# Kernel tuning notes

Hardware: AMD Instinct MI355X
Metric: run time of the kernel (lower is better)

The kernel has to match this reference:

```python
import jax, jax.numpy as jnp
import numpy as np

B, S, TEXT_DIM, VISION_DIM, HIDDEN, HEADS = 4, 2048, 768, 768, 512, 8
HEAD_DIM = HIDDEN // HEADS


def setup_inputs() -> dict:
    key = jax.random.key(0)
    ks = jax.random.split(key, 9)
    s_in = 1.0 / np.sqrt(TEXT_DIM)
    s_h = 1.0 / np.sqrt(HIDDEN)
    return {
        "text_embeds": jax.random.normal(ks[0], (B, S, TEXT_DIM), dtype=jnp.float32),
        "Wq": jax.random.uniform(ks[1], (TEXT_DIM, HIDDEN), jnp.float32, -s_in, s_in),
        "bq": jax.random.uniform(ks[2], (HIDDEN,), jnp.float32, -s_in, s_in),
        "Wk": jax.random.uniform(ks[3], (TEXT_DIM, HIDDEN), jnp.float32, -s_in, s_in),
        "bk": jax.random.uniform(ks[4], (HIDDEN,), jnp.float32, -s_in, s_in),
        "Wv": jax.random.uniform(ks[5], (TEXT_DIM, HIDDEN), jnp.float32, -s_in, s_in),
        "bv": jax.random.uniform(ks[6], (HIDDEN,), jnp.float32, -s_in, s_in),
        "Wo": jax.random.uniform(ks[7], (HIDDEN, VISION_DIM), jnp.float32, -s_h, s_h),
        "bo": jax.random.uniform(ks[8], (VISION_DIM,), jnp.float32, -s_h, s_h),
    }


def reference(text_embeds, Wq, bq, Wk, bk, Wv, bv, Wo, bo):
    b, s, _ = text_embeds.shape
    # QKV projections -> [b, heads, s, head_dim]
    def proj(W, bias):
        y = jnp.einsum("bsd,dh->bsh", text_embeds, W) + bias
        return y.reshape(b, s, HEADS, HEAD_DIM).transpose(0, 2, 1, 3)
    q, k, v = proj(Wq, bq), proj(Wk, bk), proj(Wv, bv)
    scores = jnp.einsum("bhqd,bhkd->bhqk", q, k) / np.sqrt(HEAD_DIM).astype(np.float32)
    weights = jax.nn.softmax(scores, axis=-1)
    attended = jnp.einsum("bhqk,bhkd->bhqd", weights, v)
    attended = attended.transpose(0, 2, 1, 3).reshape(b, s, HIDDEN)
    out = jnp.einsum("bsh,hv->bsv", attended, Wo) + bo
    return jnp.squeeze(out, axis=1) if out.shape[1] == 1 else out
```

## Files before the change

### kernel.cpp

```cpp
#include <hip/hip_runtime.h>
#include <hip/hip_bf16.h>

#define BATCH 4
#define SEQ 2048
#define TDIM 768
#define VDIM 768
#define HID 512
#define NHEADS 8
#define HDIM 64
#define MROWS (BATCH * SEQ)
#define NQKV (3 * HID)

typedef unsigned short ushort_t;
typedef __attribute__((ext_vector_type(8))) short short8;
typedef __attribute__((ext_vector_type(4))) short short4v;
typedef __attribute__((ext_vector_type(4))) float floatx4;

#define QSCALE 0.18033688011112042f

__device__ __forceinline__ ushort_t bf16_rne(float f) {
    unsigned int u = __float_as_uint(f);
    u = (u + 0x7fffu + ((u >> 16) & 1u)) >> 16;
    return (ushort_t)u;
}

__device__ __forceinline__ void async16(const ushort_t* g, ushort_t* l) {
    __builtin_amdgcn_global_load_lds(
        (const __attribute__((address_space(1))) unsigned int*)g,
        (__attribute__((address_space(3))) unsigned int*)l, 16, 0, 0);
}

__global__ __launch_bounds__(256) void conv_x(const float* __restrict__ X,
                                              ushort_t* __restrict__ Xb)
{
    const int i = (blockIdx.x * 256 + threadIdx.x) * 4;
    const floatx4 v = *(const floatx4*)(X + i);
    short4v o;
#pragma unroll
    for (int j = 0; j < 4; ++j) o[j] = (short)bf16_rne(v[j]);
    *(short4v*)(Xb + i) = o;
}

__global__ __launch_bounds__(256) void transp_w(
    const float* __restrict__ Wq, const float* __restrict__ Wk,
    const float* __restrict__ Wv, const float* __restrict__ Wo,
    ushort_t* __restrict__ Wqkvt, ushort_t* __restrict__ Wot)
{
    __shared__ float tile[32][33];
    const int z = blockIdx.z;
    const float* src;
    ushort_t* dst;
    int R, C;
    if (z < 3) {
        src = (z == 0) ? Wq : (z == 1) ? Wk : Wv;
        dst = Wqkvt + (size_t)z * HID * TDIM;
        R = TDIM; C = HID;
    } else {
        src = Wo; dst = Wot; R = HID; C = VDIM;
    }
    const int tx = threadIdx.x & 31, ty = threadIdx.x >> 5;
    const int c0 = blockIdx.x * 32, r0 = blockIdx.y * 32;
    if (c0 >= C || r0 >= R) return;
#pragma unroll
    for (int i = 0; i < 4; ++i)
        tile[ty + i * 8][tx] = src[(size_t)(r0 + ty + i * 8) * C + c0 + tx];
    __syncthreads();
#pragma unroll
    for (int i = 0; i < 4; ++i)
        dst[(size_t)(c0 + ty + i * 8) * R + r0 + tx] = bf16_rne(tile[tx][ty + i * 8]);
}

template<int KD, bool SWAPPED>
__device__ __forceinline__ void gemm128(
    const ushort_t* __restrict__ A, const ushort_t* __restrict__ Bt,
    int m0, int n0, ushort_t* As, ushort_t* Bs, floatx4 (&acc)[4][4])
{
    const int tid  = threadIdx.x;
    const int lane = tid & 63;
    const int w    = tid >> 6;
    const int l15  = lane & 15;
    const int quad = lane >> 4;
    const int wrow = w >> 1;
    const int wcol = w & 1;

    const int srow = lane >> 3;
    const int scol = (lane & 7) * 8;

    const ushort_t* ga = A  + (size_t)(m0 + w * 32 + srow) * KD + scol;
    const ushort_t* gb = Bt + (size_t)(n0 + w * 32 + srow) * KD + scol;
    ushort_t* la = As + (w * 32) * 64;
    ushort_t* lb = Bs + (w * 32) * 64;

    for (int kt = 0; kt < KD; kt += 64) {
#pragma unroll
        for (int i = 0; i < 4; ++i) {
            async16(ga + (size_t)(i * 8) * KD + kt, la + i * 8 * 64);
            async16(gb + (size_t)(i * 8) * KD + kt, lb + i * 8 * 64);
        }
        __syncthreads();
#pragma unroll
        for (int half = 0; half < 2; ++half) {
            const int kk = half * 32 + quad * 8;
            short8 af[4], bf[4];
#pragma unroll
            for (int t = 0; t < 4; ++t) {
                af[t] = *(const short8*)&As[(wrow * 64 + t * 16 + l15) * 64 + kk];
                bf[t] = *(const short8*)&Bs[(wcol * 64 + t * 16 + l15) * 64 + kk];
            }
#pragma unroll
            for (int mi = 0; mi < 4; ++mi)
#pragma unroll
                for (int ni = 0; ni < 4; ++ni) {
                    if (SWAPPED)
                        acc[mi][ni] = __builtin_amdgcn_mfma_f32_16x16x32_bf16(
                            bf[ni], af[mi], acc[mi][ni], 0, 0, 0);
                    else
                        acc[mi][ni] = __builtin_amdgcn_mfma_f32_16x16x32_bf16(
                            af[mi], bf[ni], acc[mi][ni], 0, 0, 0);
                }
        }
        __syncthreads();
    }
}

__global__ __launch_bounds__(256) void qkv_gemm_mfma(
    const ushort_t* __restrict__ Xb, const ushort_t* __restrict__ Wt,
    const float* __restrict__ bq, const float* __restrict__ bk,
    const float* __restrict__ bv,
    ushort_t* __restrict__ Q, ushort_t* __restrict__ K, ushort_t* __restrict__ V)
{
    __shared__ __align__(16) ushort_t As[128 * 64];
    __shared__ __align__(16) ushort_t Bs[128 * 64];

    const int bx = blockIdx.x;
    const int m0 = blockIdx.y * 128;
    const int n0 = bx * 128;
    const int which = bx >> 2;
    const bool isV = (which == 2);

    floatx4 acc[4][4];
#pragma unroll
    for (int i = 0; i < 4; ++i)
#pragma unroll
        for (int j = 0; j < 4; ++j) acc[i][j] = (floatx4)0.0f;

    if (isV) gemm128<TDIM, false>(Xb, Wt, m0, n0, As, Bs, acc);
    else     gemm128<TDIM, true >(Xb, Wt, m0, n0, As, Bs, acc);

    const int lane = threadIdx.x & 63;
    const int w    = threadIdx.x >> 6;
    const int l15  = lane & 15;
    const int quad = lane >> 4;
    const int wrow = w >> 1;
    const int wcol = w & 1;

    if (!isV) {
        const float* bias = (which == 0) ? bq : bk;
        const float scale = (which == 0) ? QSCALE : 1.0f;
        ushort_t* Out = (which == 0) ? Q : K;
#pragma unroll
        for (int mi = 0; mi < 4; ++mi) {
            const int m = m0 + wrow * 64 + mi * 16 + l15;
            const int b = m >> 11;
            const int s = m & 2047;
#pragma unroll
            for (int ni = 0; ni < 4; ++ni) {
                const int c = (n0 - which * HID) + wcol * 64 + ni * 16 + quad * 4;
                const int h = c >> 6;
                const int d0 = c & 63;
                const floatx4 b4 = *(const floatx4*)(bias + c);
                short4v pk;
#pragma unroll
                for (int r = 0; r < 4; ++r)
                    pk[r] = (short)bf16_rne((acc[mi][ni][r] + b4[r]) * scale);
                *(short4v*)&Out[((size_t)(b * NHEADS + h) * SEQ + s) * HDIM + d0] = pk;
            }
        }
    } else {
#pragma unroll
        for (int ni = 0; ni < 4; ++ni) {
            const int c = (n0 - 2 * HID) + wcol * 64 + ni * 16 + l15;
            const int h = c >> 6;
            const int d = c & 63;
            const float b1 = bv[c];
#pragma unroll
            for (int mi = 0; mi < 4; ++mi) {
                const int mb = m0 + wrow * 64 + mi * 16 + quad * 4;
                const int b = mb >> 11;
                const int s0 = mb & 2047;
                short4v pk;
#pragma unroll
                for (int r = 0; r < 4; ++r)
                    pk[r] = (short)bf16_rne(acc[mi][ni][r] + b1);
                *(short4v*)&V[((size_t)(b * NHEADS + h) * HDIM + d) * SEQ + s0] = pk;
            }
        }
    }
}

#define KSTR 72
#define PSTR 72

__global__ __launch_bounds__(256) void flash_attn_mfma(
    const ushort_t* __restrict__ Q, const ushort_t* __restrict__ K,
    const ushort_t* __restrict__ Vt, ushort_t* __restrict__ Att)
{
    __shared__ __align__(16) ushort_t Ks[2][64 * KSTR];
    __shared__ __align__(16) ushort_t Vs[2][64 * KSTR];
    __shared__ __align__(16) ushort_t Ps[4][32 * PSTR];

    const int tid  = threadIdx.x;
    const int lane = tid & 63;
    const int w    = tid >> 6;
    const int l15  = lane & 15;
    const int quad = lane >> 4;

    const int bh = blockIdx.x;
    const int b  = bh >> 3;
    const int h  = bh & 7;
    const int q0 = blockIdx.y * 128;

    const ushort_t* Qb = Q  + (size_t)bh * SEQ * HDIM;
    const ushort_t* Kb = K  + (size_t)bh * SEQ * HDIM;
    const ushort_t* Vb = Vt + (size_t)bh * HDIM * SEQ;

    short8 qfA0, qfA1, qfB0, qfB1;
    {
        const ushort_t* qa = Qb + (size_t)(q0 + w * 32 + l15) * HDIM + quad * 8;
        const ushort_t* qb2 = qa + 16 * HDIM;
        qfA0 = *(const short8*)(qa);
        qfA1 = *(const short8*)(qa + 32);
        qfB0 = *(const short8*)(qb2);
        qfB1 = *(const short8*)(qb2 + 32);
    }

    float lA = 0.f, lB = 0.f;
    floatx4 ofA[4], ofB[4];
#pragma unroll
    for (int t = 0; t < 4; ++t) { ofA[t] = (floatx4)0.0f; ofB[t] = (floatx4)0.0f; }

    const int srow = tid >> 3;
    const int sseg = (tid & 7) * 8;

    const ushort_t* gk = Kb + (size_t)srow * HDIM + sseg;
    const ushort_t* gv = Vb + (size_t)srow * SEQ + sseg;
    const int lofs = srow * KSTR + sseg;

    short8 kr0 = *(const short8*)(gk);
    short8 kr1 = *(const short8*)(gk + (size_t)32 * HDIM);
    short8 vr0 = *(const short8*)(gv);
    short8 vr1 = *(const short8*)(gv + (size_t)32 * SEQ);

    int buf = 0;
    for (int kt = 0; kt < SEQ; kt += 64) {
        *(short8*)&Ks[buf][lofs]             = kr0;
        *(short8*)&Ks[buf][lofs + 32 * KSTR] = kr1;
        *(short8*)&Vs[buf][lofs]             = vr0;
        *(short8*)&Vs[buf][lofs + 32 * KSTR] = vr1;
        __syncthreads();

        if (kt + 64 < SEQ) {
            kr0 = *(const short8*)(gk + (size_t)(kt + 64) * HDIM);
            kr1 = *(const short8*)(gk + (size_t)(kt + 96) * HDIM);
            vr0 = *(const short8*)(gv + (kt + 64));
            vr1 = *(const short8*)(gv + (size_t)32 * SEQ + (kt + 64));
        }

        floatx4 saccA[4], saccB[4];
#pragma unroll
        for (int t = 0; t < 4; ++t) {
            const short8 kf0 = *(const short8*)&Ks[buf][(t * 16 + l15) * KSTR + quad * 8];
            const short8 kf1 = *(const short8*)&Ks[buf][(t * 16 + l15) * KSTR + 32 + quad * 8];
            floatx4 a = (floatx4)0.0f, bb = (floatx4)0.0f;
            a  = __builtin_amdgcn_mfma_f32_16x16x32_bf16(kf0, qfA0, a, 0, 0, 0);
            a  = __builtin_amdgcn_mfma_f32_16x16x32_bf16(kf1, qfA1, a, 0, 0, 0);
            bb = __builtin_amdgcn_mfma_f32_16x16x32_bf16(kf0, qfB0, bb, 0, 0, 0);
            bb = __builtin_amdgcn_mfma_f32_16x16x32_bf16(kf1, qfB1, bb, 0, 0, 0);
            saccA[t] = a;
            saccB[t] = bb;
        }

        float rsA = 0.f, rsB = 0.f;
#pragma unroll
        for (int t = 0; t < 4; ++t) {
            float pa[4], pb[4];
#pragma unroll
            for (int r = 0; r < 4; ++r) {
                pa[r] = exp2f(saccA[t][r]); rsA += pa[r];
                pb[r] = exp2f(saccB[t][r]); rsB += pb[r];
            }
            {
                const unsigned u0 = __float_as_uint(pa[0]) + 0x8000u;
                const unsigned u1 = __float_as_uint(pa[1]) + 0x8000u;
                const unsigned u2 = __float_as_uint(pa[2]) + 0x8000u;
                const unsigned u3 = __float_as_uint(pa[3]) + 0x8000u;
                const unsigned lo = __builtin_amdgcn_perm(u1, u0, 0x07060302u);
                const unsigned hi = __builtin_amdgcn_perm(u3, u2, 0x07060302u);
                *(unsigned long long*)&Ps[w][l15 * PSTR + t * 16 + quad * 4] =
                    ((unsigned long long)hi << 32) | lo;
            }
            {
                const unsigned u0 = __float_as_uint(pb[0]) + 0x8000u;
                const unsigned u1 = __float_as_uint(pb[1]) + 0x8000u;
                const unsigned u2 = __float_as_uint(pb[2]) + 0x8000u;
                const unsigned u3 = __float_as_uint(pb[3]) + 0x8000u;
                const unsigned lo = __builtin_amdgcn_perm(u1, u0, 0x07060302u);
                const unsigned hi = __builtin_amdgcn_perm(u3, u2, 0x07060302u);
                *(unsigned long long*)&Ps[w][(16 + l15) * PSTR + t * 16 + quad * 4] =
                    ((unsigned long long)hi << 32) | lo;
            }
        }
        lA += rsA;
        lB += rsB;
        asm volatile("s_waitcnt lgkmcnt(0)" ::: "memory");

        const short8 pfA0 = *(const short8*)&Ps[w][l15 * PSTR + quad * 8];
        const short8 pfA1 = *(const short8*)&Ps[w][l15 * PSTR + 32 + quad * 8];
        const short8 pfB0 = *(const short8*)&Ps[w][(16 + l15) * PSTR + quad * 8];
        const short8 pfB1 = *(const short8*)&Ps[w][(16 + l15) * PSTR + 32 + quad * 8];

#pragma unroll
        for (int t = 0; t < 4; ++t) {
            const short8 vf0 = *(const short8*)&Vs[buf][(t * 16 + l15) * KSTR + quad * 8];
            const short8 vf1 = *(const short8*)&Vs[buf][(t * 16 + l15) * KSTR + 32 + quad * 8];
            ofA[t] = __builtin_amdgcn_mfma_f32_16x16x32_bf16(vf0, pfA0, ofA[t], 0, 0, 0);
            ofA[t] = __builtin_amdgcn_mfma_f32_16x16x32_bf16(vf1, pfA1, ofA[t], 0, 0, 0);
            ofB[t] = __builtin_amdgcn_mfma_f32_16x16x32_bf16(vf0, pfB0, ofB[t], 0, 0, 0);
            ofB[t] = __builtin_amdgcn_mfma_f32_16x16x32_bf16(vf1, pfB1, ofB[t], 0, 0, 0);
        }
        buf ^= 1;
    }

    lA += __shfl_xor(lA, 16); lA += __shfl_xor(lA, 32);
    lB += __shfl_xor(lB, 16); lB += __shfl_xor(lB, 32);
    const float invA = 1.f / lA;
    const float invB = 1.f / lB;

    const int sA = q0 + w * 32 + l15;
    ushort_t* arowA = Att + ((size_t)(b * SEQ + sA)) * HID + h * HDIM;
    ushort_t* arowB = arowA + (size_t)16 * HID;
#pragma unroll
    for (int t = 0; t < 4; ++t) {
        short4v pkA, pkB;
#pragma unroll
        for (int r = 0; r < 4; ++r) {
            pkA[r] = (short)bf16_rne(ofA[t][r] * invA);
            pkB[r] = (short)bf16_rne(ofB[t][r] * invB);
        }
        *(short4v*)&arowA[t * 16 + quad * 4] = pkA;
        *(short4v*)&arowB[t * 16 + quad * 4] = pkB;
    }
}

__global__ __launch_bounds__(256) void out_gemm_mfma(
    const ushort_t* __restrict__ Attb, const ushort_t* __restrict__ Wot,
    const float* __restrict__ bo, float* __restrict__ Y)
{
    __shared__ __align__(16) ushort_t As[128 * 64];
    __shared__ __align__(16) ushort_t Bs[128 * 64];

    const int m0 = blockIdx.y * 128;
    const int n0 = blockIdx.x * 128;

    floatx4 acc[4][4];
#pragma unroll
    for (int i = 0; i < 4; ++i)
#pragma unroll
        for (int j = 0; j < 4; ++j) acc[i][j] = (floatx4)0.0f;

    gemm128<HID, true>(Attb, Wot, m0, n0, As, Bs, acc);

    const int lane = threadIdx.x & 63;
    const int w    = threadIdx.x >> 6;
    const int l15  = lane & 15;
    const int quad = lane >> 4;
    const int wrow = w >> 1;
    const int wcol = w & 1;

#pragma unroll
    for (int mi = 0; mi < 4; ++mi) {
        const int m = m0 + wrow * 64 + mi * 16 + l15;
#pragma unroll
        for (int ni = 0; ni < 4; ++ni) {
            const int nb = n0 + wcol * 64 + ni * 16 + quad * 4;
            const floatx4 b4 = *(const floatx4*)(bo + nb);
            floatx4 o;
#pragma unroll
            for (int r = 0; r < 4; ++r) o[r] = acc[mi][ni][r] + b4[r];
            *(floatx4*)&Y[(size_t)m * VDIM + nb] = o;
        }
    }
}

extern "C" void kernel_launch(void* const* d_in, const int* in_sizes, int n_in,
                              void* d_out, int out_size, void* d_ws, size_t ws_size,
                              hipStream_t stream)
{
    const float* text = (const float*)d_in[0];
    const float* Wq = (const float*)d_in[1];
    const float* bq = (const float*)d_in[2];
    const float* Wk = (const float*)d_in[3];
    const float* bk = (const float*)d_in[4];
    const float* Wv = (const float*)d_in[5];
    const float* bv = (const float*)d_in[6];
    const float* Wo = (const float*)d_in[7];
    const float* bo = (const float*)d_in[8];
    float* out = (float*)d_out;

    ushort_t* Xb    = (ushort_t*)d_ws;
    ushort_t* Wqkvt = Xb + (size_t)MROWS * TDIM;
    ushort_t* Wot   = Wqkvt + (size_t)NQKV * TDIM;
    ushort_t* Qw    = Wot + (size_t)VDIM * HID;
    ushort_t* Kw    = Qw + (size_t)MROWS * HID;
    ushort_t* Vtw   = Kw + (size_t)MROWS * HID;
    ushort_t* Attb  = Vtw + (size_t)MROWS * HID;

    conv_x<<<dim3(MROWS * TDIM / 1024), 256, 0, stream>>>(text, Xb);
    transp_w<<<dim3(24, 24, 4), 256, 0, stream>>>(Wq, Wk, Wv, Wo, Wqkvt, Wot);
    qkv_gemm_mfma<<<dim3(12, 64), 256, 0, stream>>>(Xb, Wqkvt, bq, bk, bv, Qw, Kw, Vtw);
    flash_attn_mfma<<<dim3(32, 16), 256, 0, stream>>>(Qw, Kw, Vtw, Attb);
    out_gemm_mfma<<<dim3(6, 64), 256, 0, stream>>>(Attb, Wot, bo, out);
}
```

Baseline: 220.7 us.

## Split key range across two wave groups in flash attention with swizzled LDS

The attention kernel now runs 512 threads per block. Two groups of four waves each process half of every 128-key chunk for the same 128 queries, and their partial outputs and row sums are combined through LDS at the end. The padded LDS layouts for K, V and P are replaced by XOR-swizzled unpadded layouts to avoid bank conflicts, and the K/V staging drops double buffering in favour of a sync before each store. This doubles in-flight waves and MFMA parallelism per block, at the cost of an extra barrier per iteration and a final cross-group reduction.

```diff
diff --git a/kernel.cpp b/kernel.cpp
--- a/kernel.cpp
+++ b/kernel.cpp
@@ -198,22 +198,23 @@
     }
 }
 
-#define KSTR 72
-#define PSTR 72
-
-__global__ __launch_bounds__(256) void flash_attn_mfma(
+#define FA_LDS_V 8192
+#define FA_LDS_P 16384
+
+__global__ __launch_bounds__(512, 4) void flash_attn_mfma(
     const ushort_t* __restrict__ Q, const ushort_t* __restrict__ K,
     const ushort_t* __restrict__ Vt, ushort_t* __restrict__ Att)
 {
-    __shared__ __align__(16) ushort_t Ks[2][64 * KSTR];
-    __shared__ __align__(16) ushort_t Vs[2][64 * KSTR];
-    __shared__ __align__(16) ushort_t Ps[4][32 * PSTR];
+    __shared__ __align__(16) ushort_t lds[32768];
 
     const int tid  = threadIdx.x;
     const int lane = tid & 63;
     const int w    = tid >> 6;
+    const int wg   = w >> 2;
+    const int wq   = w & 3;
     const int l15  = lane & 15;
     const int quad = lane >> 4;
+    const int key  = l15 & 7;
 
     const int bh = blockIdx.x;
     const int b  = bh >> 3;
@@ -226,12 +227,11 @@
 
     short8 qfA0, qfA1, qfB0, qfB1;
     {
-        const ushort_t* qa = Qb + (size_t)(q0 + w * 32 + l15) * HDIM + quad * 8;
-        const ushort_t* qb2 = qa + 16 * HDIM;
+        const ushort_t* qa = Qb + (size_t)(q0 + wq * 32 + l15) * HDIM + quad * 8;
         qfA0 = *(const short8*)(qa);
         qfA1 = *(const short8*)(qa + 32);
-        qfB0 = *(const short8*)(qb2);
-        qfB1 = *(const short8*)(qb2 + 32);
+        qfB0 = *(const short8*)(qa + 16 * HDIM);
+        qfB1 = *(const short8*)(qa + 16 * HDIM + 32);
     }
 
     float lA = 0.f, lB = 0.f;
@@ -239,38 +239,50 @@
 #pragma unroll
     for (int t = 0; t < 4; ++t) { ofA[t] = (floatx4)0.0f; ofB[t] = (floatx4)0.0f; }
 
-    const int srow = tid >> 3;
-    const int sseg = (tid & 7) * 8;
-
-    const ushort_t* gk = Kb + (size_t)srow * HDIM + sseg;
-    const ushort_t* gv = Vb + (size_t)srow * SEQ + sseg;
-    const int lofs = srow * KSTR + sseg;
-
-    short8 kr0 = *(const short8*)(gk);
-    short8 kr1 = *(const short8*)(gk + (size_t)32 * HDIM);
-    short8 vr0 = *(const short8*)(gv);
-    short8 vr1 = *(const short8*)(gv + (size_t)32 * SEQ);
-
-    int buf = 0;
-    for (int kt = 0; kt < SEQ; kt += 64) {
-        *(short8*)&Ks[buf][lofs]             = kr0;
-        *(short8*)&Ks[buf][lofs + 32 * KSTR] = kr1;
-        *(short8*)&Vs[buf][lofs]             = vr0;
-        *(short8*)&Vs[buf][lofs + 32 * KSTR] = vr1;
+    const int krow = tid >> 3;
+    const int kg   = tid & 7;
+    const int vrow = tid >> 4;
+    const int vg   = tid & 15;
+
+    const ushort_t* gK = Kb + (size_t)krow * HDIM + kg * 8;
+    const ushort_t* gV = Vb + (size_t)vrow * SEQ + vg * 8;
+
+    const int ka0 = krow * 64 + (kg ^ (krow & 7)) * 8;
+    const int ka1 = ka0 + 64 * 64;
+    const int va0 = FA_LDS_V + vrow * 128 + (((vg & 7) ^ (vrow & 7)) | (vg & 8)) * 8;
+    const int va1 = va0 + 32 * 128;
+
+    short8 kr0 = *(const short8*)(gK);
+    short8 kr1 = *(const short8*)(gK + (size_t)64 * HDIM);
+    short8 vr0 = *(const short8*)(gV);
+    short8 vr1 = *(const short8*)(gV + (size_t)32 * SEQ);
+
+    ushort_t* Pw = lds + FA_LDS_P + w * 2048;
+    const int kkrow0 = wg * 64;
+    const int vgb    = wg * 8;
+
+    for (int it = 0; it < 16; ++it) {
+        if (it) __syncthreads();
+        *(short8*)&lds[ka0] = kr0;
+        *(short8*)&lds[ka1] = kr1;
+        *(short8*)&lds[va0] = vr0;
+        *(short8*)&lds[va1] = vr1;
         __syncthreads();
 
-        if (kt + 64 < SEQ) {
-            kr0 = *(const short8*)(gk + (size_t)(kt + 64) * HDIM);
-            kr1 = *(const short8*)(gk + (size_t)(kt + 96) * HDIM);
-            vr0 = *(const short8*)(gv + (kt + 64));
-            vr1 = *(const short8*)(gv + (size_t)32 * SEQ + (kt + 64));
+        if (it < 15) {
+            const int kt = (it + 1) * 128;
+            kr0 = *(const short8*)(gK + (size_t)kt * HDIM);
+            kr1 = *(const short8*)(gK + (size_t)(kt + 64) * HDIM);
+            vr0 = *(const short8*)(gV + kt);
+            vr1 = *(const short8*)(gV + (size_t)32 * SEQ + kt);
         }
 
         floatx4 saccA[4], saccB[4];
 #pragma unroll
         for (int t = 0; t < 4; ++t) {
-            const short8 kf0 = *(const short8*)&Ks[buf][(t * 16 + l15) * KSTR + quad * 8];
-            const short8 kf1 = *(const short8*)&Ks[buf][(t * 16 + l15) * KSTR + 32 + quad * 8];
+            const int rbase = (kkrow0 + t * 16 + l15) * 64;
+            const short8 kf0 = *(const short8*)&lds[rbase + (quad ^ key) * 8];
+            const short8 kf1 = *(const short8*)&lds[rbase + ((quad + 4) ^ key) * 8];
             floatx4 a = (floatx4)0.0f, bb = (floatx4)0.0f;
             a  = __builtin_amdgcn_mfma_f32_16x16x32_bf16(kf0, qfA0, a, 0, 0, 0);
             a  = __builtin_amdgcn_mfma_f32_16x16x32_bf16(kf1, qfA1, a, 0, 0, 0);
@@ -289,6 +301,7 @@
                 pa[r] = exp2f(saccA[t][r]); rsA += pa[r];
                 pb[r] = exp2f(saccB[t][r]); rsB += pb[r];
             }
+            const int pofs = ((2 * t + (quad >> 1)) ^ key) * 8 + (quad & 1) * 4;
             {
                 const unsigned u0 = __float_as_uint(pa[0]) + 0x8000u;
                 const unsigned u1 = __float_as_uint(pa[1]) + 0x8000u;
@@ -296,7 +309,7 @@
                 const unsigned u3 = __float_as_uint(pa[3]) + 0x8000u;
                 const unsigned lo = __builtin_amdgcn_perm(u1, u0, 0x07060302u);
                 const unsigned hi = __builtin_amdgcn_perm(u3, u2, 0x07060302u);
-                *(unsigned long long*)&Ps[w][l15 * PSTR + t * 16 + quad * 4] =
+                *(unsigned long long*)&Pw[l15 * 64 + pofs] =
                     ((unsigned long long)hi << 32) | lo;
             }
             {
@@ -306,7 +319,7 @@
                 const unsigned u3 = __float_as_uint(pb[3]) + 0x8000u;
                 const unsigned lo = __builtin_amdgcn_perm(u1, u0, 0x07060302u);
                 const unsigned hi = __builtin_amdgcn_perm(u3, u2, 0x07060302u);
-                *(unsigned long long*)&Ps[w][(16 + l15) * PSTR + t * 16 + quad * 4] =
+                *(unsigned long long*)&Pw[(16 + l15) * 64 + pofs] =
                     ((unsigned long long)hi << 32) | lo;
             }
         }
@@ -314,41 +327,70 @@
         lB += rsB;
         asm volatile("s_waitcnt lgkmcnt(0)" ::: "memory");
 
-        const short8 pfA0 = *(const short8*)&Ps[w][l15 * PSTR + quad * 8];
-        const short8 pfA1 = *(const short8*)&Ps[w][l15 * PSTR + 32 + quad * 8];
-        const short8 pfB0 = *(const short8*)&Ps[w][(16 + l15) * PSTR + quad * 8];
-        const short8 pfB1 = *(const short8*)&Ps[w][(16 + l15) * PSTR + 32 + quad * 8];
+        const short8 pfA0 = *(const short8*)&Pw[l15 * 64 + (quad ^ key) * 8];
+        const short8 pfA1 = *(const short8*)&Pw[l15 * 64 + ((quad + 4) ^ key) * 8];
+        const short8 pfB0 = *(const short8*)&Pw[(16 + l15) * 64 + (quad ^ key) * 8];
+        const short8 pfB1 = *(const short8*)&Pw[(16 + l15) * 64 + ((quad + 4) ^ key) * 8];
 
 #pragma unroll
         for (int t = 0; t < 4; ++t) {
-            const short8 vf0 = *(const short8*)&Vs[buf][(t * 16 + l15) * KSTR + quad * 8];
-            const short8 vf1 = *(const short8*)&Vs[buf][(t * 16 + l15) * KSTR + 32 + quad * 8];
+            const int vbase = FA_LDS_V + (t * 16 + l15) * 128;
+            const short8 vf0 = *(const short8*)&lds[vbase + (vgb | (quad ^ key)) * 8];
+            const short8 vf1 = *(const short8*)&lds[vbase + (vgb | ((quad + 4) ^ key)) * 8];
             ofA[t] = __builtin_amdgcn_mfma_f32_16x16x32_bf16(vf0, pfA0, ofA[t], 0, 0, 0);
             ofA[t] = __builtin_amdgcn_mfma_f32_16x16x32_bf16(vf1, pfA1, ofA[t], 0, 0, 0);
             ofB[t] = __builtin_amdgcn_mfma_f32_16x16x32_bf16(vf0, pfB0, ofB[t], 0, 0, 0);
             ofB[t] = __builtin_amdgcn_mfma_f32_16x16x32_bf16(vf1, pfB1, ofB[t], 0, 0, 0);
         }
-        buf ^= 1;
     }
 
     lA += __shfl_xor(lA, 16); lA += __shfl_xor(lA, 32);
     lB += __shfl_xor(lB, 16); lB += __shfl_xor(lB, 32);
-    const float invA = 1.f / lA;
-    const float invB = 1.f / lB;
-
-    const int sA = q0 + w * 32 + l15;
-    ushort_t* arowA = Att + ((size_t)(b * SEQ + sA)) * HID + h * HDIM;
-    ushort_t* arowB = arowA + (size_t)16 * HID;
-#pragma unroll
-    for (int t = 0; t < 4; ++t) {
-        short4v pkA, pkB;
-#pragma unroll
-        for (int r = 0; r < 4; ++r) {
-            pkA[r] = (short)bf16_rne(ofA[t][r] * invA);
-            pkB[r] = (short)bf16_rne(ofB[t][r] * invB);
-        }
-        *(short4v*)&arowA[t * 16 + quad * 4] = pkA;
-        *(short4v*)&arowB[t * 16 + quad * 4] = pkB;
+
+    __syncthreads();
+    float* ex  = (float*)lds;
+    float* lex = (float*)(lds + FA_LDS_P);
+    if (wg == 1) {
+#pragma unroll
+        for (int t = 0; t < 4; ++t)
+#pragma unroll
+            for (int r = 0; r < 4; ++r) {
+                ex[(wq * 32 + t * 4 + r) * 64 + lane]      = ofA[t][r];
+                ex[(wq * 32 + 16 + t * 4 + r) * 64 + lane] = ofB[t][r];
+            }
+        if (quad == 0) {
+            lex[wq * 32 + l15]      = lA;
+            lex[wq * 32 + 16 + l15] = lB;
+        }
+    }
+    __syncthreads();
+    if (wg == 0) {
+#pragma unroll
+        for (int t = 0; t < 4; ++t)
+#pragma unroll
+            for (int r = 0; r < 4; ++r) {
+                ofA[t][r] += ex[(wq * 32 + t * 4 + r) * 64 + lane];
+                ofB[t][r] += ex[(wq * 32 + 16 + t * 4 + r) * 64 + lane];
+            }
+        lA += lex[wq * 32 + l15];
+        lB += lex[wq * 32 + 16 + l15];
+        const float invA = 1.f / lA;
+        const float invB = 1.f / lB;
+
+        const int sA = q0 + wq * 32 + l15;
+        ushort_t* arowA = Att + ((size_t)(b * SEQ + sA)) * HID + h * HDIM;
+        ushort_t* arowB = arowA + (size_t)16 * HID;
+#pragma unroll
+        for (int t = 0; t < 4; ++t) {
+            short4v pkA, pkB;
+#pragma unroll
+            for (int r = 0; r < 4; ++r) {
+                pkA[r] = (short)bf16_rne(ofA[t][r] * invA);
+                pkB[r] = (short)bf16_rne(ofB[t][r] * invB);
+            }
+            *(short4v*)&arowA[t * 16 + quad * 4] = pkA;
+            *(short4v*)&arowB[t * 16 + quad * 4] = pkB;
+        }
     }
 }
 
@@ -418,6 +460,6 @@
     conv_x<<<dim3(MROWS * TDIM / 1024), 256, 0, stream>>>(text, Xb);
     transp_w<<<dim3(24, 24, 4), 256, 0, stream>>>(Wq, Wk, Wv, Wo, Wqkvt, Wot);
     qkv_gemm_mfma<<<dim3(12, 64), 256, 0, stream>>>(Xb, Wqkvt, bq, bk, bv, Qw, Kw, Vtw);
-    flash_attn_mfma<<<dim3(32, 16), 256, 0, stream>>>(Qw, Kw, Vtw, Attb);
+    flash_attn_mfma<<<dim3(32, 16), 512, 0, stream>>>(Qw, Kw, Vtw, Attb);
     out_gemm_mfma<<<dim3(6, 64), 256, 0, stream>>>(Attb, Wot, bo, out);
 }
```

Result: slower. 231.8 us (+5.0%).

## Split attention over key halves, swizzle LDS, and add a combine kernel

Applied to the files above, without the earlier changes.

The flash attention kernel now splits the key sequence into two halves across a new grid dimension, uses 512-thread blocks covering 256 queries, and writes unnormalized partial outputs plus row sums. A new combine kernel sums the two halves and normalizes them into the attention buffer, which reuses the Xb workspace. LDS tiles drop row padding in favour of XOR swizzling to avoid bank conflicts and shrink shared memory. This gives more blocks and more parallelism per head, at the cost of an extra kernel launch, extra global traffic for the partial outputs, and bf16 rounding of those partials.

```diff
diff --git a/kernel.cpp b/kernel.cpp
--- a/kernel.cpp
+++ b/kernel.cpp
@@ -22,6 +22,10 @@
     unsigned int u = __float_as_uint(f);
     u = (u + 0x7fffu + ((u >> 16) & 1u)) >> 16;
     return (ushort_t)u;
+}
+
+__device__ __forceinline__ float bf16_to_f(ushort_t v) {
+    return __uint_as_float(((unsigned)v) << 16);
 }
 
 __device__ __forceinline__ void async16(const ushort_t* g, ushort_t* l) {
@@ -198,40 +202,38 @@
     }
 }
 
-#define KSTR 72
-#define PSTR 72
-
-__global__ __launch_bounds__(256) void flash_attn_mfma(
+__global__ __launch_bounds__(512) void flash_attn_mfma(
     const ushort_t* __restrict__ Q, const ushort_t* __restrict__ K,
-    const ushort_t* __restrict__ Vt, ushort_t* __restrict__ Att)
-{
-    __shared__ __align__(16) ushort_t Ks[2][64 * KSTR];
-    __shared__ __align__(16) ushort_t Vs[2][64 * KSTR];
-    __shared__ __align__(16) ushort_t Ps[4][32 * PSTR];
+    const ushort_t* __restrict__ Vt, ushort_t* __restrict__ Opart,
+    float* __restrict__ Lpart)
+{
+    __shared__ __align__(16) ushort_t lds[32768];
 
     const int tid  = threadIdx.x;
     const int lane = tid & 63;
     const int w    = tid >> 6;
     const int l15  = lane & 15;
     const int quad = lane >> 4;
+    const int key  = l15 & 7;
 
     const int bh = blockIdx.x;
     const int b  = bh >> 3;
     const int h  = bh & 7;
-    const int q0 = blockIdx.y * 128;
+    const int q0 = blockIdx.y * 256;
+    const int z  = blockIdx.z;
+    const int kk0 = z * (SEQ / 2);
 
     const ushort_t* Qb = Q  + (size_t)bh * SEQ * HDIM;
-    const ushort_t* Kb = K  + (size_t)bh * SEQ * HDIM;
-    const ushort_t* Vb = Vt + (size_t)bh * HDIM * SEQ;
+    const ushort_t* Kb = K  + (size_t)bh * SEQ * HDIM + (size_t)kk0 * HDIM;
+    const ushort_t* Vb = Vt + (size_t)bh * HDIM * SEQ + kk0;
 
     short8 qfA0, qfA1, qfB0, qfB1;
     {
         const ushort_t* qa = Qb + (size_t)(q0 + w * 32 + l15) * HDIM + quad * 8;
-        const ushort_t* qb2 = qa + 16 * HDIM;
         qfA0 = *(const short8*)(qa);
         qfA1 = *(const short8*)(qa + 32);
-        qfB0 = *(const short8*)(qb2);
-        qfB1 = *(const short8*)(qb2 + 32);
+        qfB0 = *(const short8*)(qa + 16 * HDIM);
+        qfB1 = *(const short8*)(qa + 16 * HDIM + 32);
     }
 
     float lA = 0.f, lB = 0.f;
@@ -240,37 +242,33 @@
     for (int t = 0; t < 4; ++t) { ofA[t] = (floatx4)0.0f; ofB[t] = (floatx4)0.0f; }
 
     const int srow = tid >> 3;
-    const int sseg = (tid & 7) * 8;
-
-    const ushort_t* gk = Kb + (size_t)srow * HDIM + sseg;
-    const ushort_t* gv = Vb + (size_t)srow * SEQ + sseg;
-    const int lofs = srow * KSTR + sseg;
-
-    short8 kr0 = *(const short8*)(gk);
-    short8 kr1 = *(const short8*)(gk + (size_t)32 * HDIM);
-    short8 vr0 = *(const short8*)(gv);
-    short8 vr1 = *(const short8*)(gv + (size_t)32 * SEQ);
-
-    int buf = 0;
-    for (int kt = 0; kt < SEQ; kt += 64) {
-        *(short8*)&Ks[buf][lofs]             = kr0;
-        *(short8*)&Ks[buf][lofs + 32 * KSTR] = kr1;
-        *(short8*)&Vs[buf][lofs]             = vr0;
-        *(short8*)&Vs[buf][lofs + 32 * KSTR] = vr1;
+    const int sg   = tid & 7;
+    const ushort_t* gK = Kb + (size_t)srow * HDIM + sg * 8;
+    const ushort_t* gV = Vb + (size_t)srow * SEQ + sg * 8;
+    const int sofs = srow * 64 + (sg ^ (srow & 7)) * 8;
+
+    ushort_t* Pw = lds + 16384 + w * 2048;
+
+    short8 kr = *(const short8*)(gK);
+    short8 vr = *(const short8*)(gV);
+
+    for (int it = 0; it < 16; ++it) {
+        const int buf = it & 1;
+        *(short8*)&lds[buf * 4096 + sofs]        = kr;
+        *(short8*)&lds[8192 + buf * 4096 + sofs] = vr;
         __syncthreads();
 
-        if (kt + 64 < SEQ) {
-            kr0 = *(const short8*)(gk + (size_t)(kt + 64) * HDIM);
-            kr1 = *(const short8*)(gk + (size_t)(kt + 96) * HDIM);
-            vr0 = *(const short8*)(gv + (kt + 64));
-            vr1 = *(const short8*)(gv + (size_t)32 * SEQ + (kt + 64));
+        if (it < 15) {
+            kr = *(const short8*)(gK + (size_t)(it + 1) * 64 * HDIM);
+            vr = *(const short8*)(gV + (it + 1) * 64);
         }
 
         floatx4 saccA[4], saccB[4];
 #pragma unroll
         for (int t = 0; t < 4; ++t) {
-            const short8 kf0 = *(const short8*)&Ks[buf][(t * 16 + l15) * KSTR + quad * 8];
-            const short8 kf1 = *(const short8*)&Ks[buf][(t * 16 + l15) * KSTR + 32 + quad * 8];
+            const int kb = buf * 4096 + (t * 16 + l15) * 64;
+            const short8 kf0 = *(const short8*)&lds[kb + (quad ^ key) * 8];
+            const short8 kf1 = *(const short8*)&lds[kb + ((quad + 4) ^ key) * 8];
             floatx4 a = (floatx4)0.0f, bb = (floatx4)0.0f;
             a  = __builtin_amdgcn_mfma_f32_16x16x32_bf16(kf0, qfA0, a, 0, 0, 0);
             a  = __builtin_amdgcn_mfma_f32_16x16x32_bf16(kf1, qfA1, a, 0, 0, 0);
@@ -289,6 +287,7 @@
                 pa[r] = exp2f(saccA[t][r]); rsA += pa[r];
                 pb[r] = exp2f(saccB[t][r]); rsB += pb[r];
             }
+            const int pofs = ((2 * t + (quad >> 1)) ^ key) * 8 + (quad & 1) * 4;
             {
                 const unsigned u0 = __float_as_uint(pa[0]) + 0x8000u;
                 const unsigned u1 = __float_as_uint(pa[1]) + 0x8000u;
@@ -296,7 +295,7 @@
                 const unsigned u3 = __float_as_uint(pa[3]) + 0x8000u;
                 const unsigned lo = __builtin_amdgcn_perm(u1, u0, 0x07060302u);
                 const unsigned hi = __builtin_amdgcn_perm(u3, u2, 0x07060302u);
-                *(unsigned long long*)&Ps[w][l15 * PSTR + t * 16 + quad * 4] =
+                *(unsigned long long*)&Pw[l15 * 64 + pofs] =
                     ((unsigned long long)hi << 32) | lo;
             }
             {
@@ -306,7 +305,7 @@
                 const unsigned u3 = __float_as_uint(pb[3]) + 0x8000u;
                 const unsigned lo = __builtin_amdgcn_perm(u1, u0, 0x07060302u);
                 const unsigned hi = __builtin_amdgcn_perm(u3, u2, 0x07060302u);
-                *(unsigned long long*)&Ps[w][(16 + l15) * PSTR + t * 16 + quad * 4] =
+                *(unsigned long long*)&Pw[(16 + l15) * 64 + pofs] =
                     ((unsigned long long)hi << 32) | lo;
             }
         }
@@ -314,42 +313,72 @@
         lB += rsB;
         asm volatile("s_waitcnt lgkmcnt(0)" ::: "memory");
 
-        const short8 pfA0 = *(const short8*)&Ps[w][l15 * PSTR + quad * 8];
-        const short8 pfA1 = *(const short8*)&Ps[w][l15 * PSTR + 32 + quad * 8];
-        const short8 pfB0 = *(const short8*)&Ps[w][(16 + l15) * PSTR + quad * 8];
-        const short8 pfB1 = *(const short8*)&Ps[w][(16 + l15) * PSTR + 32 + quad * 8];
+        const short8 pfA0 = *(const short8*)&Pw[l15 * 64 + (quad ^ key) * 8];
+        const short8 pfA1 = *(const short8*)&Pw[l15 * 64 + ((quad + 4) ^ key) * 8];
+        const short8 pfB0 = *(const short8*)&Pw[(16 + l15) * 64 + (quad ^ key) * 8];
+        const short8 pfB1 = *(const short8*)&Pw[(16 + l15) * 64 + ((quad + 4) ^ key) * 8];
 
 #pragma unroll
         for (int t = 0; t < 4; ++t) {
-            const short8 vf0 = *(const short8*)&Vs[buf][(t * 16 + l15) * KSTR + quad * 8];
-            const short8 vf1 = *(const short8*)&Vs[buf][(t * 16 + l15) * KSTR + 32 + quad * 8];
+            const int vb2 = 8192 + buf * 4096 + (t * 16 + l15) * 64;
+            const short8 vf0 = *(const short8*)&lds[vb2 + (quad ^ key) * 8];
+            const short8 vf1 = *(const short8*)&lds[vb2 + ((quad + 4) ^ key) * 8];
             ofA[t] = __builtin_amdgcn_mfma_f32_16x16x32_bf16(vf0, pfA0, ofA[t], 0, 0, 0);
             ofA[t] = __builtin_amdgcn_mfma_f32_16x16x32_bf16(vf1, pfA1, ofA[t], 0, 0, 0);
             ofB[t] = __builtin_amdgcn_mfma_f32_16x16x32_bf16(vf0, pfB0, ofB[t], 0, 0, 0);
             ofB[t] = __builtin_amdgcn_mfma_f32_16x16x32_bf16(vf1, pfB1, ofB[t], 0, 0, 0);
         }
-        buf ^= 1;
     }
 
     lA += __shfl_xor(lA, 16); lA += __shfl_xor(lA, 32);
     lB += __shfl_xor(lB, 16); lB += __shfl_xor(lB, 32);
-    const float invA = 1.f / lA;
-    const float invB = 1.f / lB;
 
     const int sA = q0 + w * 32 + l15;
-    ushort_t* arowA = Att + ((size_t)(b * SEQ + sA)) * HID + h * HDIM;
+    ushort_t* arowA = Opart + (size_t)z * MROWS * HID
+                    + ((size_t)(b * SEQ + sA)) * HID + h * HDIM;
     ushort_t* arowB = arowA + (size_t)16 * HID;
 #pragma unroll
     for (int t = 0; t < 4; ++t) {
         short4v pkA, pkB;
 #pragma unroll
         for (int r = 0; r < 4; ++r) {
-            pkA[r] = (short)bf16_rne(ofA[t][r] * invA);
-            pkB[r] = (short)bf16_rne(ofB[t][r] * invB);
+            pkA[r] = (short)bf16_rne(ofA[t][r]);
+            pkB[r] = (short)bf16_rne(ofB[t][r]);
         }
         *(short4v*)&arowA[t * 16 + quad * 4] = pkA;
         *(short4v*)&arowB[t * 16 + quad * 4] = pkB;
     }
+    if (quad == 0) {
+        Lpart[(size_t)(z * 32 + bh) * SEQ + sA]      = lA;
+        Lpart[(size_t)(z * 32 + bh) * SEQ + sA + 16] = lB;
+    }
+}
+
+__global__ __launch_bounds__(256) void combine_halves(
+    const ushort_t* __restrict__ Opart, const float* __restrict__ Lpart,
+    ushort_t* __restrict__ Att)
+{
+    const int idx = blockIdx.x * 256 + threadIdx.x;
+    const int m  = idx >> 6;
+    const int c0 = (idx & 63) * 8;
+    const int b = m >> 11;
+    const int s = m & 2047;
+    const int h = c0 >> 6;
+    const int bh = b * 8 + h;
+
+    const float l = Lpart[(size_t)bh * SEQ + s] +
+                    Lpart[(size_t)(32 + bh) * SEQ + s];
+    const float inv = 1.f / l;
+
+    const short8 o0 = *(const short8*)&Opart[(size_t)m * HID + c0];
+    const short8 o1 = *(const short8*)&Opart[(size_t)MROWS * HID + (size_t)m * HID + c0];
+    short8 o;
+#pragma unroll
+    for (int j = 0; j < 8; ++j) {
+        const float f = (bf16_to_f((ushort_t)o0[j]) + bf16_to_f((ushort_t)o1[j])) * inv;
+        o[j] = (short)bf16_rne(f);
+    }
+    *(short8*)&Att[(size_t)m * HID + c0] = o;
 }
 
 __global__ __launch_bounds__(256) void out_gemm_mfma(
@@ -413,11 +442,14 @@
     ushort_t* Qw    = Wot + (size_t)VDIM * HID;
     ushort_t* Kw    = Qw + (size_t)MROWS * HID;
     ushort_t* Vtw   = Kw + (size_t)MROWS * HID;
-    ushort_t* Attb  = Vtw + (size_t)MROWS * HID;
+    ushort_t* Opart = Vtw + (size_t)MROWS * HID;
+    float*    Lpart = (float*)(Opart + (size_t)2 * MROWS * HID);
+    ushort_t* Attb  = Xb;
 
     conv_x<<<dim3(MROWS * TDIM / 1024), 256, 0, stream>>>(text, Xb);
     transp_w<<<dim3(24, 24, 4), 256, 0, stream>>>(Wq, Wk, Wv, Wo, Wqkvt, Wot);
     qkv_gemm_mfma<<<dim3(12, 64), 256, 0, stream>>>(Xb, Wqkvt, bq, bk, bv, Qw, Kw, Vtw);
-    flash_attn_mfma<<<dim3(32, 16), 256, 0, stream>>>(Qw, Kw, Vtw, Attb);
+    flash_attn_mfma<<<dim3(32, 8, 2), 512, 0, stream>>>(Qw, Kw, Vtw, Opart, Lpart);
+    combine_halves<<<dim3(MROWS * HID / 8 / 256), 256, 0, stream>>>(Opart, Lpart, Attb);
     out_gemm_mfma<<<dim3(6, 64), 256, 0, stream>>>(Attb, Wot, bo, out);
 }
```

Measured after the change: 214.4 us. 1.03x faster.
